# Kernel tuning notes

Hardware: AMD Instinct MI355X
Metric: run time of the kernel (lower is better)

Reference implementation:

```python
import jax, jax.numpy as jnp
import numpy as np

N_NODES = 100000
N_EDGES = 1600000
N_GRAPHS = 512
F_IN = 128
HID = 128
N_CLS = 10


def setup_inputs() -> dict:
    key = jax.random.key(0)
    ks = jax.random.split(key, 12)
    x = jax.random.normal(ks[0], (N_NODES, F_IN), dtype=jnp.float32)
    edge_index = jax.random.randint(ks[1], (2, N_EDGES), 0, N_NODES, dtype=jnp.int64)
    batch = jnp.sort(jax.random.randint(ks[2], (N_NODES,), 0, N_GRAPHS, dtype=jnp.int64))
    def glorot(k, shape):
        lim = float(np.sqrt(6.0 / (shape[0] + shape[1])))
        return jax.random.uniform(k, shape, jnp.float32, -lim, lim)
    return {
        "x": x, "edge_index": edge_index, "batch": batch,
        "W1": glorot(ks[3], (F_IN, HID)), "b1": jnp.zeros((HID,), jnp.float32),
        "W2": glorot(ks[4], (HID, HID)), "b2": jnp.zeros((HID,), jnp.float32),
        "W3": glorot(ks[5], (HID, HID)), "b3": jnp.zeros((HID,), jnp.float32),
        "Wc1": glorot(ks[6], (2 * HID, HID)), "bc1": jnp.zeros((HID,), jnp.float32),
        "Wc2": glorot(ks[7], (HID, N_CLS)), "bc2": jnp.zeros((N_CLS,), jnp.float32),
    }


def _gcn_layer(h, W, b, src, dst, dinv_sqrt, norm):
    # GCNConv: transform, then symmetric-normalized aggregation with self-loops.
    h = h @ W                                    # [N, HID]
    msgs = h[src] * norm[:, None]                # gather + scale  [E, HID]
    agg = jax.ops.segment_sum(msgs, dst, num_segments=N_NODES)
    agg = agg + h * (dinv_sqrt * dinv_sqrt)[:, None]   # self-loop term (1/deg)
    return jax.nn.relu(agg + b)


def reference(x, edge_index, batch, W1, b1, W2, b2, W3, b3, Wc1, bc1, Wc2, bc2):
    src, dst = edge_index[0], edge_index[1]
    # degree including self loop (counted at aggregation target = dst)
    deg = jax.ops.segment_sum(jnp.ones((N_EDGES,), jnp.float32), dst,
                              num_segments=N_NODES) + 1.0
    dinv_sqrt = jax.lax.rsqrt(deg)
    norm = dinv_sqrt[src] * dinv_sqrt[dst]       # [E]

    h = _gcn_layer(x, W1, b1, src, dst, dinv_sqrt, norm)
    h = _gcn_layer(h, W2, b2, src, dst, dinv_sqrt, norm)
    h = _gcn_layer(h, W3, b3, src, dst, dinv_sqrt, norm)

    # mean_max pooling over graphs
    counts = jax.ops.segment_sum(jnp.ones((N_NODES,), jnp.float32), batch,
                                 num_segments=N_GRAPHS)
    sums = jax.ops.segment_sum(h, batch, num_segments=N_GRAPHS)
    g_mean = sums / jnp.maximum(counts, 1.0)[:, None]
    g_max = jax.ops.segment_max(h, batch, num_segments=N_GRAPHS)
    g_max = jnp.where(counts[:, None] > 0, g_max, 0.0)
    g = jnp.concatenate([g_mean, g_max], axis=1)  # [G, 2*HID]

    # MLP head (dropout is identity in eval mode)
    hcls = jax.nn.relu(g @ Wc1 + bc1)
    return hcls @ Wc2 + bc2                       # [G, N_CLS]
```

## Files before the change

kernel.cpp:

```cpp
#include <hip/hip_runtime.h>
#include <hip/hip_bf16.h>
#include <hip/hip_fp16.h>

#define HIDDIM 128
#define NABLK 256
#define EPB 6250
#define BCAP 5120
#define BSTRIDE 7168

typedef __attribute__((ext_vector_type(8))) _Float16 half8;
typedef __attribute__((ext_vector_type(4))) float f32x4;

__device__ __forceinline__ int scan256_incl(int v, int* sbuf, int t) {
    sbuf[t] = v;
    __syncthreads();
    for (int off = 1; off < 256; off <<= 1) {
        int x = sbuf[t];
        if (t >= off) x += sbuf[t - off];
        __syncthreads();
        sbuf[t] = x;
        __syncthreads();
    }
    return sbuf[t];
}

__global__ __launch_bounds__(1024) void k_bucketA(const int* __restrict__ ei, int E,
                                                  int2* __restrict__ sortedA,
                                                  int* __restrict__ tableA, int nbuck) {
    __shared__ int2 sEdge[EPB];
    __shared__ int hist[512];
    __shared__ int sb[512];
    int t = threadIdx.x;
    int blk = blockIdx.x;
    int base = blk * EPB;
    int cnt = min(EPB, E - base);
    if (t < 512) hist[t] = 0;
    __syncthreads();
    int es[7], ed[7], rk[7];
#pragma unroll
    for (int it = 0; it < 7; ++it) {
        int i = it * 1024 + t;
        es[it] = 0; ed[it] = -1; rk[it] = 0;
        if (i < cnt) {
            es[it] = ei[base + i];
            ed[it] = ei[E + base + i];
            rk[it] = atomicAdd(&hist[ed[it] >> 8], 1);
        }
    }
    __syncthreads();
    if (t < 512) sb[t] = hist[t];
    __syncthreads();
    for (int off = 1; off < 512; off <<= 1) {
        int x = 0;
        if (t < 512) { x = sb[t]; if (t >= off) x += sb[t - off]; }
        __syncthreads();
        if (t < 512) sb[t] = x;
        __syncthreads();
    }
#pragma unroll
    for (int it = 0; it < 7; ++it) {
        if (ed[it] >= 0) {
            int b = ed[it] >> 8;
            int slot = sb[b] - hist[b] + rk[it];
            sEdge[slot] = make_int2(es[it], ed[it]);
        }
    }
    if (t <= nbuck) tableA[t * NABLK + blk] = sb[t] - hist[t];
    __syncthreads();
    for (int j = t; j < cnt; j += 1024) sortedA[base + j] = sEdge[j];
}

__global__ __launch_bounds__(256) void k_bucketB(const int2* __restrict__ sortedA,
                                                 const int* __restrict__ tableA,
                                                 int* __restrict__ csr_src,
                                                 int2* __restrict__ row2,
                                                 float* __restrict__ dinv, int N) {
    __shared__ int2 eIn[BCAP];
    __shared__ int h[256];
    __shared__ int cur[256];
    __shared__ int scanbuf[256];
    int b = blockIdx.x;
    int t = threadIdx.x;
    int s = tableA[b * NABLK + t];
    int c = tableA[(b + 1) * NABLK + t] - s;
    int rIncl = scan256_incl(c, scanbuf, t);
    int rOff = rIncl - c;
    int nE = scanbuf[255];
    for (int k = 0; k < c; ++k) {
        int p = rOff + k;
        if (p < BCAP) eIn[p] = sortedA[t * EPB + s + k];
    }
    h[t] = 0;
    __syncthreads();
    if (nE > BCAP) nE = BCAP;
    for (int j = t; j < nE; j += 256) atomicAdd(&h[eIn[j].y & 255], 1);
    __syncthreads();
    int deg = h[t];
    int pdeg = (deg + 7) & ~7;
    int pIncl = scan256_incl(pdeg, scanbuf, t);
    int pOff = pIncl - pdeg;
    int g = b * 256 + t;
    int gbase = b * BSTRIDE;
    if (g < N) {
        dinv[g] = rsqrtf((float)deg + 1.0f);
        row2[g] = make_int2(gbase + pOff, pdeg);
    }
    cur[t] = pOff;
    __syncthreads();
    for (int j = t; j < nE; j += 256) {
        int2 e = eIn[j];
        int sl = atomicAdd(&cur[e.y & 255], 1);
        csr_src[gbase + sl] = e.x;
    }
    for (int j = deg; j < pdeg; ++j) csr_src[gbase + pOff + j] = N;
}

__global__ __launch_bounds__(256) void k_wprep(const float* __restrict__ W1,
                                               const float* __restrict__ W2,
                                               const float* __restrict__ W3,
                                               __half* __restrict__ Whf,
                                               __half* __restrict__ Wdf) {
    int layer = blockIdx.x;
    const float* W = layer == 0 ? W1 : (layer == 1 ? W2 : W3);
    __half* oh = Whf + (size_t)layer * 16384;
    __half* od = Wdf + (size_t)layer * 16384;
    int t = threadIdx.x;
#pragma unroll
    for (int i = 0; i < 8; ++i) {
        int fr = t * 8 + i;
        int kk = fr >> 9;
        int jt = (fr >> 6) & 7;
        int lane = fr & 63;
        int col = jt * 16 + (lane & 15);
        int kbase = kk * 32 + ((lane >> 4) << 3);
        __half hv[8], dv[8];
#pragma unroll
        for (int e = 0; e < 8; ++e) {
            float v = W[(kbase + e) * 128 + col];
            __half h = __float2half_rn(v);
            hv[e] = h;
            dv[e] = __float2half_rn(v - __half2float(h));
        }
        *(uint4*)(oh + (size_t)fr * 8) = *(uint4*)hv;
        *(uint4*)(od + (size_t)fr * 8) = *(uint4*)dv;
    }
}

__global__ __launch_bounds__(256) void k_gemm1(const float* __restrict__ A,
                                               const __half* __restrict__ Bh,
                                               const __half* __restrict__ Bd,
                                               const float* __restrict__ dinv,
                                               __half* __restrict__ Oh, int nrows) {
    int wave = threadIdx.x >> 6, lane = threadIdx.x & 63;
    int row0 = blockIdx.x * 64 + wave * 16;
    int arow = row0 + (lane & 15);
    if (arow >= nrows) arow = nrows - 1;
    int kg = lane >> 4;
    const float* ap = A + (size_t)arow * 128 + kg * 8;
    f32x4 acc[8];
#pragma unroll
    for (int j = 0; j < 8; ++j) acc[j] = (f32x4){0.f, 0.f, 0.f, 0.f};
#pragma unroll
    for (int kk = 0; kk < 4; ++kk) {
        float4 a0 = *(const float4*)(ap + kk * 32);
        float4 a1 = *(const float4*)(ap + kk * 32 + 4);
        float av[8] = {a0.x, a0.y, a0.z, a0.w, a1.x, a1.y, a1.z, a1.w};
        half8 ah, da;
#pragma unroll
        for (int e = 0; e < 8; ++e) {
            _Float16 h = (_Float16)av[e];
            ah[e] = h;
            da[e] = (_Float16)(av[e] - (float)h);
        }
        const half8* bhp = (const half8*)(Bh + ((size_t)(kk * 8) * 64 + lane) * 8);
        const half8* bdp = (const half8*)(Bd + ((size_t)(kk * 8) * 64 + lane) * 8);
#pragma unroll
        for (int jt = 0; jt < 8; ++jt) {
            half8 bh = bhp[jt * 64];
            half8 bd = bdp[jt * 64];
            acc[jt] = __builtin_amdgcn_mfma_f32_16x16x32_f16(ah, bh, acc[jt], 0, 0, 0);
            acc[jt] = __builtin_amdgcn_mfma_f32_16x16x32_f16(da, bh, acc[jt], 0, 0, 0);
            acc[jt] = __builtin_amdgcn_mfma_f32_16x16x32_f16(ah, bd, acc[jt], 0, 0, 0);
        }
    }
    int ocol = lane & 15;
    int orow_base = row0 + (lane >> 4) * 4;
#pragma unroll
    for (int r = 0; r < 4; ++r) {
        int orow = orow_base + r;
        if (orow < nrows) {
            float dv = dinv[orow];
#pragma unroll
            for (int jt = 0; jt < 8; ++jt)
                Oh[(size_t)orow * 128 + jt * 16 + ocol] = __float2half_rn(acc[jt][r] * dv);
        }
    }
}

__global__ __launch_bounds__(256) void k_gemm16(const __half* __restrict__ A,
                                                const __half* __restrict__ Bh,
                                                const __half* __restrict__ Bd,
                                                const float* __restrict__ dinv,
                                                __half* __restrict__ Oh, int nrows) {
    int wave = threadIdx.x >> 6, lane = threadIdx.x & 63;
    int row0 = blockIdx.x * 64 + wave * 16;
    int arow = row0 + (lane & 15);
    if (arow >= nrows) arow = nrows - 1;
    int kg = lane >> 4;
    const __half* ap = A + (size_t)arow * 128 + kg * 8;
    f32x4 acc[8];
#pragma unroll
    for (int j = 0; j < 8; ++j) acc[j] = (f32x4){0.f, 0.f, 0.f, 0.f};
#pragma unroll
    for (int kk = 0; kk < 4; ++kk) {
        half8 ah = *(const half8*)(ap + kk * 32);
        const half8* bhp = (const half8*)(Bh + ((size_t)(kk * 8) * 64 + lane) * 8);
        const half8* bdp = (const half8*)(Bd + ((size_t)(kk * 8) * 64 + lane) * 8);
#pragma unroll
        for (int jt = 0; jt < 8; ++jt) {
            half8 bh = bhp[jt * 64];
            half8 bd = bdp[jt * 64];
            acc[jt] = __builtin_amdgcn_mfma_f32_16x16x32_f16(ah, bh, acc[jt], 0, 0, 0);
            acc[jt] = __builtin_amdgcn_mfma_f32_16x16x32_f16(ah, bd, acc[jt], 0, 0, 0);
        }
    }
    int ocol = lane & 15;
    int orow_base = row0 + (lane >> 4) * 4;
#pragma unroll
    for (int r = 0; r < 4; ++r) {
        int orow = orow_base + r;
        if (orow < nrows) {
            float dv = dinv[orow];
#pragma unroll
            for (int jt = 0; jt < 8; ++jt)
                Oh[(size_t)orow * 128 + jt * 16 + ocol] = __float2half_rn(acc[jt][r] * dv);
        }
    }
}

__global__ __launch_bounds__(256) void k_agg(const __half* __restrict__ hHs,
                                             const int2* __restrict__ row2,
                                             const int* __restrict__ csr_src,
                                             const float* __restrict__ dinv,
                                             const float* __restrict__ bias,
                                             __half* __restrict__ outH, int n) {
    int node = blockIdx.x * 4 + (threadIdx.x >> 6);
    int lane = threadIdx.x & 63;
    if (node >= n) return;
    int half = lane >> 5;
    int q = lane & 31;
    unsigned qo = (unsigned)q << 3;
    float dd = dinv[node];
    int2 ro = row2[node];
    const int* __restrict__ cp = csr_src + ro.x;
    int iters = ro.y >> 3;
    float4 acc = make_float4(0.f, 0.f, 0.f, 0.f);
    for (int it = 0; it < iters; ++it) {
        int i0 = cp[half];
        int i1 = cp[2 + half];
        int i2 = cp[4 + half];
        int i3 = cp[6 + half];
        cp += 8;
        uint2 w0 = *(const uint2*)((const char*)hHs + (((size_t)(unsigned)i0) << 8) + qo);
        uint2 w1 = *(const uint2*)((const char*)hHs + (((size_t)(unsigned)i1) << 8) + qo);
        uint2 w2 = *(const uint2*)((const char*)hHs + (((size_t)(unsigned)i2) << 8) + qo);
        uint2 w3 = *(const uint2*)((const char*)hHs + (((size_t)(unsigned)i3) << 8) + qo);
#pragma unroll
        for (int p = 0; p < 4; ++p) {
            uint2 w = p == 0 ? w0 : (p == 1 ? w1 : (p == 2 ? w2 : w3));
            float2 f0 = __half22float2(*(const __half2*)&w.x);
            float2 f1 = __half22float2(*(const __half2*)&w.y);
            acc.x += f0.x;
            acc.y += f0.y;
            acc.z += f1.x;
            acc.w += f1.y;
        }
    }
    acc.x += __shfl_xor(acc.x, 32);
    acc.y += __shfl_xor(acc.y, 32);
    acc.z += __shfl_xor(acc.z, 32);
    acc.w += __shfl_xor(acc.w, 32);
    if (half == 0) {
        uint2 sw = *(const uint2*)((const char*)hHs + ((size_t)(unsigned)node << 8) + qo);
        float2 s0 = __half22float2(*(const __half2*)&sw.x);
        float2 s1 = __half22float2(*(const __half2*)&sw.y);
        float4 bb = *(const float4*)(bias + q * 4);
        __half o[4];
        o[0] = __float2half_rn(fmaxf(fmaf(dd, acc.x + s0.x, bb.x), 0.f));
        o[1] = __float2half_rn(fmaxf(fmaf(dd, acc.y + s0.y, bb.y), 0.f));
        o[2] = __float2half_rn(fmaxf(fmaf(dd, acc.z + s1.x, bb.z), 0.f));
        o[3] = __float2half_rn(fmaxf(fmaf(dd, acc.w + s1.y, bb.w), 0.f));
        *(uint2*)(outH + (size_t)node * 128 + q * 4) = *(uint2*)o;
    }
}

__global__ void k_pool(const __half* __restrict__ h, const int* __restrict__ batch,
                       float* __restrict__ gsum, float* __restrict__ gmax,
                       int* __restrict__ gcnt, int n) {
    int t = threadIdx.x;
    int start = blockIdx.x * 64;
    if (start >= n) return;
    int end = min(start + 64, n);
    int cur = batch[start];
    float s = 0.f, m = 0.f;
    int c = 0;
    for (int i = start; i < end; ++i) {
        int g = batch[i];
        if (g != cur) {
            atomicAdd(&gsum[cur * 128 + t], s);
            atomicMax((int*)&gmax[cur * 128 + t], __float_as_int(m));
            if (t == 0) atomicAdd(&gcnt[cur], c);
            s = 0.f; m = 0.f; c = 0; cur = g;
        }
        float v = __half2float(h[(size_t)i * 128 + t]);
        s += v;
        m = fmaxf(m, v);
        c++;
    }
    atomicAdd(&gsum[cur * 128 + t], s);
    atomicMax((int*)&gmax[cur * 128 + t], __float_as_int(m));
    if (t == 0) atomicAdd(&gcnt[cur], c);
}

__global__ void k_head(const float* __restrict__ gsum, const float* __restrict__ gmax,
                       const int* __restrict__ gcnt, const float* __restrict__ Wc1,
                       const float* __restrict__ bc1, const float* __restrict__ Wc2,
                       const float* __restrict__ bc2, float* __restrict__ out, int G) {
    __shared__ float gv[256];
    __shared__ float hc[128];
    int g = blockIdx.x;
    if (g >= G) return;
    int t = threadIdx.x;
    float c = (float)gcnt[g];
    float inv = 1.0f / fmaxf(c, 1.0f);
    gv[t] = gsum[g * 128 + t] * inv;
    gv[128 + t] = gmax[g * 128 + t];
    __syncthreads();
    float a = bc1[t];
#pragma unroll 8
    for (int k = 0; k < 256; ++k) a = fmaf(gv[k], Wc1[k * 128 + t], a);
    hc[t] = fmaxf(a, 0.f);
    __syncthreads();
    if (t < 10) {
        float o = bc2[t];
        for (int k = 0; k < 128; ++k) o = fmaf(hc[k], Wc2[k * 10 + t], o);
        out[g * 10 + t] = o;
    }
}

extern "C" void kernel_launch(void* const* d_in, const int* in_sizes, int n_in,
                              void* d_out, int out_size, void* d_ws, size_t ws_size,
                              hipStream_t stream) {
    const float* x   = (const float*)d_in[0];
    const int*   ei  = (const int*)d_in[1];
    const int*   bat = (const int*)d_in[2];
    const float* W1  = (const float*)d_in[3];
    const float* b1  = (const float*)d_in[4];
    const float* W2  = (const float*)d_in[5];
    const float* b2  = (const float*)d_in[6];
    const float* W3  = (const float*)d_in[7];
    const float* b3  = (const float*)d_in[8];
    const float* Wc1 = (const float*)d_in[9];
    const float* bc1 = (const float*)d_in[10];
    const float* Wc2 = (const float*)d_in[11];
    const float* bc2 = (const float*)d_in[12];
    float* out = (float*)d_out;

    const int N = in_sizes[0] / HIDDIM;
    const int E = in_sizes[1] / 2;
    const int G = out_size / 10;
    const int nbuck = (N + 255) >> 8;

    char* ws = (char*)d_ws;
    size_t off = 0;
    auto take = [&](size_t bytes) -> char* {
        char* p = ws + off;
        off += (bytes + 255) & ~(size_t)255;
        return p;
    };
    __half* aggH    = (__half*)take((size_t)N * HIDDIM * 2);
    int2*  sortedA  = (int2*)aggH;
    __half* hHs     = (__half*)take(((size_t)N + 1) * HIDDIM * 2);
    float* dinv     = (float*)take((size_t)N * 4);
    int2*  row2     = (int2*)take((size_t)N * 8);
    int*   tableA   = (int*)take((size_t)(nbuck + 1) * NABLK * 4);
    int*   csr_src  = (int*)take((size_t)nbuck * BSTRIDE * 4);
    float* gsum     = (float*)take((size_t)G * HIDDIM * 4);
    float* gmax     = (float*)take((size_t)G * HIDDIM * 4);
    int*   gcnt     = (int*)take((size_t)G * 4);
    __half* Whf     = (__half*)take((size_t)3 * 16384 * 2);
    __half* Wdf     = (__half*)take((size_t)3 * 16384 * 2);

    hipMemsetAsync(gsum, 0, (size_t)G * HIDDIM * 4, stream);
    hipMemsetAsync(gmax, 0, (size_t)G * HIDDIM * 4, stream);
    hipMemsetAsync(gcnt, 0, (size_t)G * 4, stream);
    hipMemsetAsync(hHs + (size_t)N * HIDDIM, 0, HIDDIM * 2, stream);

    k_bucketA<<<NABLK, 1024, 0, stream>>>(ei, E, sortedA, tableA, nbuck);
    k_bucketB<<<nbuck, 256, 0, stream>>>(sortedA, tableA, csr_src, row2, dinv, N);
    k_wprep<<<3, 256, 0, stream>>>(W1, W2, W3, Whf, Wdf);

    int gb = (N + 63) / 64;
    int ab = (N + 3) / 4;
    k_gemm1<<<gb, 256, 0, stream>>>(x, Whf, Wdf, dinv, hHs, N);
    k_agg<<<ab, 256, 0, stream>>>(hHs, row2, csr_src, dinv, b1, aggH, N);
    k_gemm16<<<gb, 256, 0, stream>>>(aggH, Whf + 16384, Wdf + 16384, dinv, hHs, N);
    k_agg<<<ab, 256, 0, stream>>>(hHs, row2, csr_src, dinv, b2, aggH, N);
    k_gemm16<<<gb, 256, 0, stream>>>(aggH, Whf + 32768, Wdf + 32768, dinv, hHs, N);
    k_agg<<<ab, 256, 0, stream>>>(hHs, row2, csr_src, dinv, b3, aggH, N);

    k_pool<<<(N + 63) / 64, 128, 0, stream>>>(aggH, bat, gsum, gmax, gcnt, N);
    k_head<<<G, 128, 0, stream>>>(gsum, gmax, gcnt, Wc1, bc1, Wc2, bc2, out, G);
}
```

Baseline: 354.4 us.

## Split node features into eight column slabs for cache-local aggregation

Node features are stored as eight 16-column fp16 slabs instead of row-major rows. Aggregation blocks now handle a single slab, so the random gathers for each pass touch a 3.2MB working set that can stay in L2. The GEMMs and the pooling kernel are updated to read and write the slab layout, and the three memsets are merged into one. In exchange, every source index is re-read eight times, each gather moves only 32 bytes, and the GEMM stores become strided across slabs.

```diff
diff --git a/kernel.cpp b/kernel.cpp
--- a/kernel.cpp
+++ b/kernel.cpp
@@ -119,12 +119,17 @@
                                                const float* __restrict__ W2,
                                                const float* __restrict__ W3,
                                                __half* __restrict__ Whf,
-                                               __half* __restrict__ Wdf) {
+                                               __half* __restrict__ Wdf,
+                                               __half* __restrict__ hS, int N) {
     int layer = blockIdx.x;
+    int t = threadIdx.x;
+    if (layer == 0 && t < 128) {
+        int s = t >> 4, c = t & 15;
+        hS[((size_t)s * (N + 1) + N) * 16 + c] = __float2half_rn(0.f);
+    }
     const float* W = layer == 0 ? W1 : (layer == 1 ? W2 : W3);
     __half* oh = Whf + (size_t)layer * 16384;
     __half* od = Wdf + (size_t)layer * 16384;
-    int t = threadIdx.x;
 #pragma unroll
     for (int i = 0; i < 8; ++i) {
         int fr = t * 8 + i;
@@ -150,7 +155,7 @@
                                                const __half* __restrict__ Bh,
                                                const __half* __restrict__ Bd,
                                                const float* __restrict__ dinv,
-                                               __half* __restrict__ Oh, int nrows) {
+                                               __half* __restrict__ OS, int nrows) {
     int wave = threadIdx.x >> 6, lane = threadIdx.x & 63;
     int row0 = blockIdx.x * 64 + wave * 16;
     int arow = row0 + (lane & 15);
@@ -192,28 +197,28 @@
             float dv = dinv[orow];
 #pragma unroll
             for (int jt = 0; jt < 8; ++jt)
-                Oh[(size_t)orow * 128 + jt * 16 + ocol] = __float2half_rn(acc[jt][r] * dv);
-        }
-    }
-}
-
-__global__ __launch_bounds__(256) void k_gemm16(const __half* __restrict__ A,
+                OS[((size_t)jt * (nrows + 1) + orow) * 16 + ocol] = __float2half_rn(acc[jt][r] * dv);
+        }
+    }
+}
+
+__global__ __launch_bounds__(256) void k_gemm16(const __half* __restrict__ AS,
                                                 const __half* __restrict__ Bh,
                                                 const __half* __restrict__ Bd,
                                                 const float* __restrict__ dinv,
-                                                __half* __restrict__ Oh, int nrows) {
+                                                __half* __restrict__ OS, int nrows) {
     int wave = threadIdx.x >> 6, lane = threadIdx.x & 63;
     int row0 = blockIdx.x * 64 + wave * 16;
     int arow = row0 + (lane & 15);
     if (arow >= nrows) arow = nrows - 1;
     int kg = lane >> 4;
-    const __half* ap = A + (size_t)arow * 128 + kg * 8;
     f32x4 acc[8];
 #pragma unroll
     for (int j = 0; j < 8; ++j) acc[j] = (f32x4){0.f, 0.f, 0.f, 0.f};
 #pragma unroll
     for (int kk = 0; kk < 4; ++kk) {
-        half8 ah = *(const half8*)(ap + kk * 32);
+        const __half* apk = AS + ((size_t)(kk * 2 + (kg >> 1)) * (nrows + 1) + arow) * 16 + (kg & 1) * 8;
+        half8 ah = *(const half8*)apk;
         const half8* bhp = (const half8*)(Bh + ((size_t)(kk * 8) * 64 + lane) * 8);
         const half8* bdp = (const half8*)(Bd + ((size_t)(kk * 8) * 64 + lane) * 8);
 #pragma unroll
@@ -233,73 +238,59 @@
             float dv = dinv[orow];
 #pragma unroll
             for (int jt = 0; jt < 8; ++jt)
-                Oh[(size_t)orow * 128 + jt * 16 + ocol] = __float2half_rn(acc[jt][r] * dv);
-        }
-    }
-}
-
-__global__ __launch_bounds__(256) void k_agg(const __half* __restrict__ hHs,
-                                             const int2* __restrict__ row2,
-                                             const int* __restrict__ csr_src,
-                                             const float* __restrict__ dinv,
-                                             const float* __restrict__ bias,
-                                             __half* __restrict__ outH, int n) {
-    int node = blockIdx.x * 4 + (threadIdx.x >> 6);
+                OS[((size_t)jt * (nrows + 1) + orow) * 16 + ocol] = __float2half_rn(acc[jt][r] * dv);
+        }
+    }
+}
+
+__global__ __launch_bounds__(1024) void k_agg(const __half* __restrict__ hS,
+                                              const int2* __restrict__ row2,
+                                              const int* __restrict__ csr_src,
+                                              const float* __restrict__ dinv,
+                                              const float* __restrict__ bias,
+                                              __half* __restrict__ outS, int N) {
+    int s = blockIdx.x & 7;
+    int node = (blockIdx.x >> 3) * 16 + (threadIdx.x >> 6);
+    if (node >= N) return;
     int lane = threadIdx.x & 63;
-    if (node >= n) return;
-    int half = lane >> 5;
-    int q = lane & 31;
-    unsigned qo = (unsigned)q << 3;
+    int eg = lane >> 3;
+    int cp2 = lane & 7;
+    const char* hs = (const char*)hS + (size_t)s * (N + 1) * 32;
+    int2 ro = row2[node];
     float dd = dinv[node];
-    int2 ro = row2[node];
-    const int* __restrict__ cp = csr_src + ro.x;
+    const int* cp = csr_src + ro.x + eg;
     int iters = ro.y >> 3;
-    float4 acc = make_float4(0.f, 0.f, 0.f, 0.f);
+    unsigned co = (unsigned)cp2 << 2;
+    float a0 = 0.f, a1 = 0.f;
     for (int it = 0; it < iters; ++it) {
-        int i0 = cp[half];
-        int i1 = cp[2 + half];
-        int i2 = cp[4 + half];
-        int i3 = cp[6 + half];
+        int idx = *cp;
         cp += 8;
-        uint2 w0 = *(const uint2*)((const char*)hHs + (((size_t)(unsigned)i0) << 8) + qo);
-        uint2 w1 = *(const uint2*)((const char*)hHs + (((size_t)(unsigned)i1) << 8) + qo);
-        uint2 w2 = *(const uint2*)((const char*)hHs + (((size_t)(unsigned)i2) << 8) + qo);
-        uint2 w3 = *(const uint2*)((const char*)hHs + (((size_t)(unsigned)i3) << 8) + qo);
-#pragma unroll
-        for (int p = 0; p < 4; ++p) {
-            uint2 w = p == 0 ? w0 : (p == 1 ? w1 : (p == 2 ? w2 : w3));
-            float2 f0 = __half22float2(*(const __half2*)&w.x);
-            float2 f1 = __half22float2(*(const __half2*)&w.y);
-            acc.x += f0.x;
-            acc.y += f0.y;
-            acc.z += f1.x;
-            acc.w += f1.y;
-        }
-    }
-    acc.x += __shfl_xor(acc.x, 32);
-    acc.y += __shfl_xor(acc.y, 32);
-    acc.z += __shfl_xor(acc.z, 32);
-    acc.w += __shfl_xor(acc.w, 32);
-    if (half == 0) {
-        uint2 sw = *(const uint2*)((const char*)hHs + ((size_t)(unsigned)node << 8) + qo);
-        float2 s0 = __half22float2(*(const __half2*)&sw.x);
-        float2 s1 = __half22float2(*(const __half2*)&sw.y);
-        float4 bb = *(const float4*)(bias + q * 4);
-        __half o[4];
-        o[0] = __float2half_rn(fmaxf(fmaf(dd, acc.x + s0.x, bb.x), 0.f));
-        o[1] = __float2half_rn(fmaxf(fmaf(dd, acc.y + s0.y, bb.y), 0.f));
-        o[2] = __float2half_rn(fmaxf(fmaf(dd, acc.z + s1.x, bb.z), 0.f));
-        o[3] = __float2half_rn(fmaxf(fmaf(dd, acc.w + s1.y, bb.w), 0.f));
-        *(uint2*)(outH + (size_t)node * 128 + q * 4) = *(uint2*)o;
-    }
-}
-
-__global__ void k_pool(const __half* __restrict__ h, const int* __restrict__ batch,
+        unsigned w = *(const unsigned*)(hs + (((size_t)(unsigned)idx) << 5) + co);
+        float2 f = __half22float2(*(const __half2*)&w);
+        a0 += f.x;
+        a1 += f.y;
+    }
+    a0 += __shfl_xor(a0, 8);  a1 += __shfl_xor(a1, 8);
+    a0 += __shfl_xor(a0, 16); a1 += __shfl_xor(a1, 16);
+    a0 += __shfl_xor(a0, 32); a1 += __shfl_xor(a1, 32);
+    if (eg == 0) {
+        unsigned sw = *(const unsigned*)(hs + (((size_t)(unsigned)node) << 5) + co);
+        float2 sf = __half22float2(*(const __half2*)&sw);
+        float2 bb = *(const float2*)(bias + s * 16 + cp2 * 2);
+        float o0 = fmaxf(fmaf(dd, a0 + sf.x, bb.x), 0.f);
+        float o1 = fmaxf(fmaf(dd, a1 + sf.y, bb.y), 0.f);
+        __half2 oh = __floats2half2_rn(o0, o1);
+        *(unsigned*)((char*)outS + (size_t)s * (N + 1) * 32 + (((size_t)(unsigned)node) << 5) + co) = *(unsigned*)&oh;
+    }
+}
+
+__global__ void k_pool(const __half* __restrict__ hSlab, const int* __restrict__ batch,
                        float* __restrict__ gsum, float* __restrict__ gmax,
                        int* __restrict__ gcnt, int n) {
     int t = threadIdx.x;
     int start = blockIdx.x * 64;
     if (start >= n) return;
+    const __half* col = hSlab + ((size_t)(t >> 4) * (n + 1)) * 16 + (t & 15);
     int end = min(start + 64, n);
     int cur = batch[start];
     float s = 0.f, m = 0.f;
@@ -312,7 +303,7 @@
             if (t == 0) atomicAdd(&gcnt[cur], c);
             s = 0.f; m = 0.f; c = 0; cur = g;
         }
-        float v = __half2float(h[(size_t)i * 128 + t]);
+        float v = __half2float(col[(size_t)i * 16]);
         s += v;
         m = fmaxf(m, v);
         c++;
@@ -378,37 +369,36 @@
         off += (bytes + 255) & ~(size_t)255;
         return p;
     };
-    __half* aggH    = (__half*)take((size_t)N * HIDDIM * 2);
-    int2*  sortedA  = (int2*)aggH;
-    __half* hHs     = (__half*)take(((size_t)N + 1) * HIDDIM * 2);
+    __half* aggS    = (__half*)take((size_t)8 * (N + 1) * 16 * 2);
+    int2*  sortedA  = (int2*)aggS;
+    __half* hS      = (__half*)take((size_t)8 * (N + 1) * 16 * 2);
     float* dinv     = (float*)take((size_t)N * 4);
     int2*  row2     = (int2*)take((size_t)N * 8);
     int*   tableA   = (int*)take((size_t)(nbuck + 1) * NABLK * 4);
     int*   csr_src  = (int*)take((size_t)nbuck * BSTRIDE * 4);
+    size_t zoff = off;
     float* gsum     = (float*)take((size_t)G * HIDDIM * 4);
     float* gmax     = (float*)take((size_t)G * HIDDIM * 4);
     int*   gcnt     = (int*)take((size_t)G * 4);
+    size_t zend = off;
     __half* Whf     = (__half*)take((size_t)3 * 16384 * 2);
     __half* Wdf     = (__half*)take((size_t)3 * 16384 * 2);
 
-    hipMemsetAsync(gsum, 0, (size_t)G * HIDDIM * 4, stream);
-    hipMemsetAsync(gmax, 0, (size_t)G * HIDDIM * 4, stream);
-    hipMemsetAsync(gcnt, 0, (size_t)G * 4, stream);
-    hipMemsetAsync(hHs + (size_t)N * HIDDIM, 0, HIDDIM * 2, stream);
+    hipMemsetAsync(ws + zoff, 0, zend - zoff, stream);
 
     k_bucketA<<<NABLK, 1024, 0, stream>>>(ei, E, sortedA, tableA, nbuck);
     k_bucketB<<<nbuck, 256, 0, stream>>>(sortedA, tableA, csr_src, row2, dinv, N);
-    k_wprep<<<3, 256, 0, stream>>>(W1, W2, W3, Whf, Wdf);
+    k_wprep<<<3, 256, 0, stream>>>(W1, W2, W3, Whf, Wdf, hS, N);
 
     int gb = (N + 63) / 64;
-    int ab = (N + 3) / 4;
-    k_gemm1<<<gb, 256, 0, stream>>>(x, Whf, Wdf, dinv, hHs, N);
-    k_agg<<<ab, 256, 0, stream>>>(hHs, row2, csr_src, dinv, b1, aggH, N);
-    k_gemm16<<<gb, 256, 0, stream>>>(aggH, Whf + 16384, Wdf + 16384, dinv, hHs, N);
-    k_agg<<<ab, 256, 0, stream>>>(hHs, row2, csr_src, dinv, b2, aggH, N);
-    k_gemm16<<<gb, 256, 0, stream>>>(aggH, Whf + 32768, Wdf + 32768, dinv, hHs, N);
-    k_agg<<<ab, 256, 0, stream>>>(hHs, row2, csr_src, dinv, b3, aggH, N);
-
-    k_pool<<<(N + 63) / 64, 128, 0, stream>>>(aggH, bat, gsum, gmax, gcnt, N);
+    int ab = ((N + 15) / 16) * 8;
+    k_gemm1<<<gb, 256, 0, stream>>>(x, Whf, Wdf, dinv, hS, N);
+    k_agg<<<ab, 1024, 0, stream>>>(hS, row2, csr_src, dinv, b1, aggS, N);
+    k_gemm16<<<gb, 256, 0, stream>>>(aggS, Whf + 16384, Wdf + 16384, dinv, hS, N);
+    k_agg<<<ab, 1024, 0, stream>>>(hS, row2, csr_src, dinv, b2, aggS, N);
+    k_gemm16<<<gb, 256, 0, stream>>>(aggS, Whf + 32768, Wdf + 32768, dinv, hS, N);
+    k_agg<<<ab, 1024, 0, stream>>>(hS, row2, csr_src, dinv, b3, aggS, N);
+
+    k_pool<<<(N + 63) / 64, 128, 0, stream>>>(aggS, bat, gsum, gmax, gcnt, N);
     k_head<<<G, 128, 0, stream>>>(gsum, gmax, gcnt, Wc1, bc1, Wc2, bc2, out, G);
 }
```

After: 859.2 us. 142% more time.

## Pool per graph via binary search and drop memsets and atomics

Applied to the files above, without the earlier changes.

Pooling now launches one block per graph. Each block binary-searches the sorted batch array to find its node range and reduces sum and max with two waves, then combines them through shared memory and writes the results directly, with no atomics. This removes the four memset launches: the sentinel row of zeros is written inside k_wprep, and the pooled buffers no longer need zero-init. It relies on batch being sorted and gives up some parallelism, since each block walks about 200 nodes serially.

```diff
diff --git a/kernel.cpp b/kernel.cpp
--- a/kernel.cpp
+++ b/kernel.cpp
@@ -119,12 +119,14 @@
                                                const float* __restrict__ W2,
                                                const float* __restrict__ W3,
                                                __half* __restrict__ Whf,
-                                               __half* __restrict__ Wdf) {
+                                               __half* __restrict__ Wdf,
+                                               __half* __restrict__ hHs, int N) {
     int layer = blockIdx.x;
+    int t = threadIdx.x;
+    if (layer == 0 && t < 128) hHs[(size_t)N * 128 + t] = __float2half_rn(0.f);
     const float* W = layer == 0 ? W1 : (layer == 1 ? W2 : W3);
     __half* oh = Whf + (size_t)layer * 16384;
     __half* od = Wdf + (size_t)layer * 16384;
-    int t = threadIdx.x;
 #pragma unroll
     for (int i = 0; i < 8; ++i) {
         int fr = t * 8 + i;
@@ -294,32 +296,38 @@
     }
 }
 
-__global__ void k_pool(const __half* __restrict__ h, const int* __restrict__ batch,
-                       float* __restrict__ gsum, float* __restrict__ gmax,
-                       int* __restrict__ gcnt, int n) {
+__global__ __launch_bounds__(128) void k_pool(const __half* __restrict__ h,
+                                              const int* __restrict__ batch,
+                                              float* __restrict__ gsum,
+                                              float* __restrict__ gmax,
+                                              int* __restrict__ gcnt, int n) {
+    int g = blockIdx.x;
     int t = threadIdx.x;
-    int start = blockIdx.x * 64;
-    if (start >= n) return;
-    int end = min(start + 64, n);
-    int cur = batch[start];
-    float s = 0.f, m = 0.f;
-    int c = 0;
-    for (int i = start; i < end; ++i) {
-        int g = batch[i];
-        if (g != cur) {
-            atomicAdd(&gsum[cur * 128 + t], s);
-            atomicMax((int*)&gmax[cur * 128 + t], __float_as_int(m));
-            if (t == 0) atomicAdd(&gcnt[cur], c);
-            s = 0.f; m = 0.f; c = 0; cur = g;
-        }
-        float v = __half2float(h[(size_t)i * 128 + t]);
-        s += v;
-        m = fmaxf(m, v);
-        c++;
-    }
-    atomicAdd(&gsum[cur * 128 + t], s);
-    atomicMax((int*)&gmax[cur * 128 + t], __float_as_int(m));
-    if (t == 0) atomicAdd(&gcnt[cur], c);
+    int wave = t >> 6, lane = t & 63;
+    int lo = 0, hi = n;
+    while (lo < hi) { int mid = (lo + hi) >> 1; if (batch[mid] < g) lo = mid + 1; else hi = mid; }
+    int lo2 = lo, hi2 = n;
+    while (lo2 < hi2) { int mid = (lo2 + hi2) >> 1; if (batch[mid] < g + 1) lo2 = mid + 1; else hi2 = mid; }
+    float s0 = 0.f, s1 = 0.f, m0 = 0.f, m1 = 0.f;
+    for (int i = lo + wave; i < lo2; i += 2) {
+        unsigned w = *(const unsigned*)(h + (size_t)i * 128 + lane * 2);
+        float2 f = __half22float2(*(const __half2*)&w);
+        s0 += f.x; s1 += f.y;
+        m0 = fmaxf(m0, f.x); m1 = fmaxf(m1, f.y);
+    }
+    __shared__ float sh[4 * 128];
+    sh[t] = s0; sh[128 + t] = s1; sh[256 + t] = m0; sh[384 + t] = m1;
+    __syncthreads();
+    if (t < 64) {
+        float2 S, M;
+        S.x = sh[t] + sh[t + 64];
+        S.y = sh[128 + t] + sh[128 + t + 64];
+        M.x = fmaxf(sh[256 + t], sh[256 + t + 64]);
+        M.y = fmaxf(sh[384 + t], sh[384 + t + 64]);
+        *(float2*)(gsum + (size_t)g * 128 + t * 2) = S;
+        *(float2*)(gmax + (size_t)g * 128 + t * 2) = M;
+        if (t == 0) gcnt[g] = lo2 - lo;
+    }
 }
 
 __global__ void k_head(const float* __restrict__ gsum, const float* __restrict__ gmax,
@@ -391,14 +399,9 @@
     __half* Whf     = (__half*)take((size_t)3 * 16384 * 2);
     __half* Wdf     = (__half*)take((size_t)3 * 16384 * 2);
 
-    hipMemsetAsync(gsum, 0, (size_t)G * HIDDIM * 4, stream);
-    hipMemsetAsync(gmax, 0, (size_t)G * HIDDIM * 4, stream);
-    hipMemsetAsync(gcnt, 0, (size_t)G * 4, stream);
-    hipMemsetAsync(hHs + (size_t)N * HIDDIM, 0, HIDDIM * 2, stream);
-
     k_bucketA<<<NABLK, 1024, 0, stream>>>(ei, E, sortedA, tableA, nbuck);
     k_bucketB<<<nbuck, 256, 0, stream>>>(sortedA, tableA, csr_src, row2, dinv, N);
-    k_wprep<<<3, 256, 0, stream>>>(W1, W2, W3, Whf, Wdf);
+    k_wprep<<<3, 256, 0, stream>>>(W1, W2, W3, Whf, Wdf, hHs, N);
 
     int gb = (N + 63) / 64;
     int ab = (N + 3) / 4;
@@ -409,6 +412,6 @@
     k_gemm16<<<gb, 256, 0, stream>>>(aggH, Whf + 32768, Wdf + 32768, dinv, hHs, N);
     k_agg<<<ab, 256, 0, stream>>>(hHs, row2, csr_src, dinv, b3, aggH, N);
 
-    k_pool<<<(N + 63) / 64, 128, 0, stream>>>(aggH, bat, gsum, gmax, gcnt, N);
+    k_pool<<<G, 128, 0, stream>>>(aggH, bat, gsum, gmax, gcnt, N);
     k_head<<<G, 128, 0, stream>>>(gsum, gmax, gcnt, Wc1, bc1, Wc2, bc2, out, G);
 }
```

New measurement: 362.7 us. 2.3% more time.
